# Performance work log

Measured on AMD Instinct MI355X. Metric: run time of the kernel, lower is better.

Reference implementation:

```python
import jax, jax.numpy as jnp
import numpy as np

B, S, C, H = 2, 2048, 2048, 16
Dh = C // H
ROPE_THETA = 10000.0


def _rope(t):
    # t: [B, S, H, Dh]; rotate-half RoPE over head_dim
    half = Dh // 2
    inv_freq = 1.0 / (ROPE_THETA ** (jnp.arange(0, half, dtype=jnp.float32) / half))
    ang = jnp.arange(S, dtype=jnp.float32)[:, None] * inv_freq[None, :]  # [S, half]
    cos = jnp.cos(ang)[None, :, None, :]  # [1,S,1,half]
    sin = jnp.sin(ang)[None, :, None, :]
    t1, t2 = t[..., :half], t[..., half:]
    return jnp.concatenate([t1 * cos - t2 * sin, t2 * cos + t1 * sin], axis=-1)


def setup_inputs() -> dict:
    key = jax.random.key(0)
    k1, k2, k3 = jax.random.split(key, 3)
    x = jax.random.normal(k1, (B, S, C), dtype=jnp.float32)
    Wqkv = jax.random.normal(k2, (C, 3 * C), dtype=jnp.float32) * (C ** -0.5)
    Wproj = jax.random.normal(k3, (C, C), dtype=jnp.float32) * (C ** -0.5)
    return {"x": x, "Wqkv": Wqkv, "Wproj": Wproj}


def reference(x, Wqkv, Wproj):
    batch, seq, hidden = x.shape
    qkv = x @ Wqkv  # [B,S,3C]
    # NOTE: torch code chunks as k, q, v (k first)
    k, q, v = jnp.split(qkv, 3, axis=-1)
    k = k.reshape(batch, seq, H, Dh)
    q = q.reshape(batch, seq, H, Dh)
    v = v.reshape(batch, seq, H, Dh)
    k = _rope(k)
    q = _rope(q)
    scale = Dh ** -0.5
    scores = jnp.einsum('bqhd,bkhd->bhqk', q, k) * scale  # [B,H,S,S]
    causal = jnp.tril(jnp.ones((seq, seq), dtype=bool))
    scores = jnp.where(causal[None, None], scores, jnp.finfo(scores.dtype).min)
    attn = jax.nn.softmax(scores, axis=-1)
    out = jnp.einsum('bhqk,bkhd->bqhd', attn, v).reshape(batch, seq, hidden)
    return out @ Wproj
```

## Files before the change

kernel.cpp:

```cpp
#include <hip/hip_runtime.h>
#include <hip/hip_bf16.h>

#define B_   2
#define S_   2048
#define C_   2048
#define H_   16
#define DH   128
#define C3   (3 * C_)

typedef __attribute__((ext_vector_type(8))) short short8;
typedef __attribute__((ext_vector_type(4))) float floatx4;

__device__ __forceinline__ void gload16(const void* g, void* l) {
  __builtin_amdgcn_global_load_lds(
      (const __attribute__((address_space(1))) unsigned int*)g,
      (__attribute__((address_space(3))) unsigned int*)l, 16, 0, 0);
}

__device__ __forceinline__ unsigned pk_bf16(float a, float b) {
  union { __hip_bfloat16 h; unsigned short u; } ua, ub;
  ua.h = __float2bfloat16(a); ub.h = __float2bfloat16(b);
  return (unsigned)ua.u | ((unsigned)ub.u << 16);
}

__device__ __forceinline__ float bf2f(short u) {
  union { unsigned u; float f; } t;
  t.u = ((unsigned)(unsigned short)u) << 16;
  return t.f;
}
__device__ __forceinline__ short f2bf(float f) {
  union { __hip_bfloat16 h; short s; } t;
  t.h = __float2bfloat16(f);
  return t.s;
}

__device__ __forceinline__ void transpose_cast_dev(
    const float* __restrict__ in, __hip_bfloat16* __restrict__ out,
    int R, int Cc, int c0, int r0, int tid, float (*tile)[33]) {
  int row = tid >> 3, col4 = tid & 7;
  float4 v = *(const float4*)&in[(size_t)(r0 + row) * Cc + c0 + col4 * 4];
  tile[row][col4 * 4 + 0] = v.x;
  tile[row][col4 * 4 + 1] = v.y;
  tile[row][col4 * 4 + 2] = v.z;
  tile[row][col4 * 4 + 3] = v.w;
  __syncthreads();
  int c = tid >> 3, r4 = tid & 7;
  union { __hip_bfloat16 b[4]; uint2 u; } t;
#pragma unroll
  for (int e = 0; e < 4; ++e) t.b[e] = __float2bfloat16(tile[r4 * 4 + e][c]);
  *(uint2*)&out[(size_t)(c0 + c) * R + r0 + r4 * 4] = t.u;
}

__global__ __launch_bounds__(256) void pre_kernel(
    const float* __restrict__ x, __hip_bfloat16* __restrict__ xb,
    const float* __restrict__ Wqkv, __hip_bfloat16* __restrict__ WqkvT) {
  __shared__ float tile[32][33];
  const int bid = blockIdx.x, tid = threadIdx.x;
  if (bid < 8192) {
    int i = bid * 256 + tid;
    float4 v = ((const float4*)x)[i];
    union { __hip_bfloat16 b[4]; uint2 u; } t;
    t.b[0] = __float2bfloat16(v.x);
    t.b[1] = __float2bfloat16(v.y);
    t.b[2] = __float2bfloat16(v.z);
    t.b[3] = __float2bfloat16(v.w);
    ((uint2*)xb)[i] = t.u;
  } else {
    int tb = bid - 8192;
    int bx = tb % 192, by = tb / 192;
    transpose_cast_dev(Wqkv, WqkvT, 2048, 6144, bx * 32, by * 32, tid, tile);
  }
}

#define S_VMCNT2 do { asm volatile("s_waitcnt vmcnt(2)" ::: "memory"); \
                      __builtin_amdgcn_sched_barrier(0); } while (0)
#define S_LGKM0  do { asm volatile("s_waitcnt lgkmcnt(0)" ::: "memory"); \
                      __builtin_amdgcn_sched_barrier(0); } while (0)
#define S_BAR    do { __builtin_amdgcn_s_barrier(); \
                      __builtin_amdgcn_sched_barrier(0); } while (0)


#define RD_A4(dst, buf, mh, sl)                                                          \
  do {                                                                                   \
    const __hip_bfloat16* base_ =                                                        \
        lds + (buf) * 28672 + (wm * 128 + (mh) * 64 + lr) * 64 + ((sl) ? sw1 : sw0);     \
    _Pragma("unroll") for (int i_ = 0; i_ < 4; ++i_)                                     \
        dst[i_] = *(const short8*)(base_ + i_ * 1024);                                   \
  } while (0)

#define RD_B3(dst, buf, sl)                                                              \
  do {                                                                                   \
    const __hip_bfloat16* base_ =                                                        \
        lds + (buf) * 28672 + 16384 + (wn * 48 + lr) * 64 + ((sl) ? sw1 : sw0);          \
    _Pragma("unroll") for (int j_ = 0; j_ < 3; ++j_)                                     \
        dst[j_] = *(const short8*)(base_ + j_ * 1024);                                   \
  } while (0)

#define MFG(afp, bfp, mh)                                                                \
  do {                                                                                   \
    __builtin_amdgcn_s_setprio(1);                                                       \
    _Pragma("unroll") for (int i_ = 0; i_ < 4; ++i_)                                     \
    _Pragma("unroll") for (int j_ = 0; j_ < 3; ++j_)                                     \
        acc[(mh) * 4 + i_][j_] = __builtin_amdgcn_mfma_f32_16x16x32_bf16(                \
            afp[i_], bfp[j_], acc[(mh) * 4 + i_][j_], 0, 0, 0);                          \
    __builtin_amdgcn_s_setprio(0);                                                       \
  } while (0)

__global__ __launch_bounds__(512, 2) void gemm1_kernel(
    const __hip_bfloat16* __restrict__ A, const __hip_bfloat16* __restrict__ Bt,
    __hip_bfloat16* __restrict__ Cp) {
  const int K = 2048;
  __shared__ __hip_bfloat16 lds[2 * 28672];
  const int tid = threadIdx.x;
  const int lane = tid & 63, wv = tid >> 6;
  const int wm = wv >> 2, wn = wv & 3;
  const int lr = lane & 15, lq = lane >> 4;
  const int m0 = blockIdx.y * 256, n0 = blockIdx.x * 192;
  const int sw0 = (lq ^ (lr & 7)) << 3;
  const int sw1 = sw0 ^ 32;

  const __hip_bfloat16* Abase = A + (size_t)m0 * K;
  const __hip_bfloat16* Bbase = Bt + (size_t)n0 * K;

  auto stA = [&](int buf, int half, int kk) {
#pragma unroll
    for (int pp = 0; pp < 2; ++pp) {
      int p = half * 2 + pp;
      int idx = p * 512 + tid;
      int row = idx >> 3;
      int lc = (idx & 7) ^ (row & 7);
      gload16(Abase + (size_t)row * K + kk + lc * 8,
              (char*)lds + buf * 57344 + p * 8192 + wv * 1024);
    }
  };
  auto stB2 = [&](int buf, int kk) {
#pragma unroll
    for (int p = 0; p < 2; ++p) {
      int idx = p * 512 + tid;
      int row = idx >> 3;
      int lc = (idx & 7) ^ (row & 7);
      gload16(Bbase + (size_t)row * K + kk + lc * 8,
              (char*)lds + buf * 57344 + 32768 + p * 8192 + wv * 1024);
    }
  };
  auto stB1 = [&](int buf, int kk) {
    int idx = 2 * 512 + tid;
    int row = idx >> 3;
    int lc = (idx & 7) ^ (row & 7);
    gload16(Bbase + (size_t)row * K + kk + lc * 8,
            (char*)lds + buf * 57344 + 49152 + wv * 1024);
  };

  floatx4 acc[8][3] = {};
  short8 afA[4], afB[4], afC[4], afD[4], bfA[3], bfB[3];

  stA(0, 0, 0); stA(0, 1, 0); stB2(0, 0); stB1(0, 0);
  stA(1, 0, 64);

#pragma unroll 1
  for (int it = 0; it < 16; ++it) {
    const int t = 2 * it;
    const int kk1 = (t + 1) * 64;
    const int kk2 = (t + 2 < 32) ? (t + 2) * 64 : 0;
    const int kk3 = (t + 3 < 32) ? (t + 3) * 64 : 0;

    S_VMCNT2; S_BAR;
    RD_A4(afA, 0, 0, 0); RD_B3(bfA, 0, 0);
    stA(1, 1, kk1);
    S_LGKM0;
    MFG(afA, bfA, 0);
    S_BAR;
    RD_A4(afB, 0, 1, 0); RD_A4(afC, 0, 0, 1);
    stB2(1, kk1);
    S_LGKM0;
    MFG(afB, bfA, 1);
    S_BAR;
    RD_B3(bfB, 0, 1); RD_A4(afD, 0, 1, 1);
    stB1(1, kk1);
    S_LGKM0;
    MFG(afC, bfB, 0);
    S_BAR;
    stA(0, 0, kk2);
    MFG(afD, bfB, 1);
    S_BAR;

    S_VMCNT2; S_BAR;
    RD_A4(afA, 1, 0, 0); RD_B3(bfA, 1, 0);
    stA(0, 1, kk2);
    S_LGKM0;
    MFG(afA, bfA, 0);
    S_BAR;
    RD_A4(afB, 1, 1, 0); RD_A4(afC, 1, 0, 1);
    stB2(0, kk2);
    S_LGKM0;
    MFG(afB, bfA, 1);
    S_BAR;
    RD_B3(bfB, 1, 1); RD_A4(afD, 1, 1, 1);
    stB1(0, kk2);
    S_LGKM0;
    MFG(afC, bfB, 0);
    S_BAR;
    stA(1, 0, kk3);
    MFG(afD, bfB, 1);
    S_BAR;
  }

  asm volatile("s_waitcnt vmcnt(0)" ::: "memory");
  __builtin_amdgcn_sched_barrier(0);

#pragma unroll
  for (int i = 0; i < 8; ++i)
#pragma unroll
    for (int j = 0; j < 3; ++j)
#pragma unroll
      for (int r = 0; r < 4; ++r) {
        int row = m0 + wm * 128 + i * 16 + lq * 4 + r;
        int col = n0 + wn * 48 + j * 16 + lr;
        Cp[(size_t)row * 6144 + col] = __float2bfloat16(acc[i][j][r]);
      }
}

#define S_VMCNT6 do { asm volatile("s_waitcnt vmcnt(6)" ::: "memory"); \
                      __builtin_amdgcn_sched_barrier(0); } while (0)

template <int NCOLS, bool OUT_F32>
__global__ __launch_bounds__(512, 2) void gemm_dp_kernel(
    const __hip_bfloat16* __restrict__ A, const __hip_bfloat16* __restrict__ Bt,
    void* __restrict__ Cp) {
  const int K = 2048, NT = 32;
  __shared__ __hip_bfloat16 lds[3 * 24576];
  const int tid = threadIdx.x;
  const int lane = tid & 63, wv = tid >> 6;
  const int wm = wv >> 1, wn = wv & 1;
  const int lr = lane & 15, lq = lane >> 4;
  const int m0 = blockIdx.y * 256, n0 = blockIdx.x * 128;
  const int sw0 = (lq ^ (lr & 7)) << 3;
  const int sw1 = sw0 ^ 32;

  auto stageA = [&](int bw, int p, int kk) {
    int idx = p * 512 + tid;
    int row = idx >> 3;
    int lc = (idx & 7) ^ (row & 7);
    gload16(A + (size_t)(m0 + row) * K + kk + lc * 8,
            (char*)lds + (size_t)bw * 49152 + (size_t)(p * 512 + wv * 64) * 16);
  };
  auto stageB = [&](int bw, int p, int kk) {
    int idx = p * 512 + tid;
    int row = idx >> 3;
    int lc = (idx & 7) ^ (row & 7);
    gload16(Bt + (size_t)(n0 + row) * K + kk + lc * 8,
            (char*)lds + (size_t)bw * 49152 + 32768 + (size_t)(p * 512 + wv * 64) * 16);
  };

#pragma unroll
  for (int p = 0; p < 4; ++p) stageA(0, p, 0);
#pragma unroll
  for (int p = 0; p < 2; ++p) stageB(0, p, 0);
#pragma unroll
  for (int p = 0; p < 4; ++p) stageA(1, p, 64);
#pragma unroll
  for (int p = 0; p < 2; ++p) stageB(1, p, 64);

  floatx4 acc[4][4] = {};
  int br = 0, bw = 2;

#pragma unroll 1
  for (int t = 0; t < NT; ++t) {
    const int kk2 = (t + 2 < NT) ? (t + 2) * 64 : 0;

    S_VMCNT6;
    S_BAR;

    const __hip_bfloat16* Ab = lds + br * 24576 + (wm * 64 + lr) * 64;
    const __hip_bfloat16* Bb = lds + br * 24576 + 16384 + (wn * 64 + lr) * 64;

    short8 af0[4], bf0[4];
#pragma unroll
    for (int i = 0; i < 4; ++i) af0[i] = *(const short8*)(Ab + i * 1024 + sw0);
#pragma unroll
    for (int j = 0; j < 4; ++j) bf0[j] = *(const short8*)(Bb + j * 1024 + sw0);
    stageA(bw, 0, kk2); stageA(bw, 1, kk2); stageB(bw, 0, kk2);
    S_LGKM0;
    __builtin_amdgcn_s_setprio(1);
#pragma unroll
    for (int i = 0; i < 4; ++i)
#pragma unroll
      for (int j = 0; j < 4; ++j)
        acc[i][j] = __builtin_amdgcn_mfma_f32_16x16x32_bf16(af0[i], bf0[j], acc[i][j], 0, 0, 0);
    __builtin_amdgcn_s_setprio(0);

    short8 af1[4], bf1[4];
#pragma unroll
    for (int i = 0; i < 4; ++i) af1[i] = *(const short8*)(Ab + i * 1024 + sw1);
#pragma unroll
    for (int j = 0; j < 4; ++j) bf1[j] = *(const short8*)(Bb + j * 1024 + sw1);
    stageA(bw, 2, kk2); stageA(bw, 3, kk2); stageB(bw, 1, kk2);
    S_LGKM0;
    __builtin_amdgcn_s_setprio(1);
#pragma unroll
    for (int i = 0; i < 4; ++i)
#pragma unroll
      for (int j = 0; j < 4; ++j)
        acc[i][j] = __builtin_amdgcn_mfma_f32_16x16x32_bf16(af1[i], bf1[j], acc[i][j], 0, 0, 0);
    __builtin_amdgcn_s_setprio(0);

    br = (br == 2) ? 0 : br + 1;
    bw = (bw == 2) ? 0 : bw + 1;
  }

  asm volatile("s_waitcnt vmcnt(0)" ::: "memory");
  __builtin_amdgcn_sched_barrier(0);

#pragma unroll
  for (int i = 0; i < 4; ++i)
#pragma unroll
    for (int j = 0; j < 4; ++j)
#pragma unroll
      for (int r = 0; r < 4; ++r) {
        int row = m0 + wm * 64 + i * 16 + lq * 4 + r;
        int col = n0 + wn * 64 + j * 16 + lr;
        if (OUT_F32)
          ((float*)Cp)[(size_t)row * NCOLS + col] = acc[i][j][r];
        else
          ((__hip_bfloat16*)Cp)[(size_t)row * NCOLS + col] = __float2bfloat16(acc[i][j][r]);
      }
}

__global__ __launch_bounds__(256) void mid_kernel(
    __hip_bfloat16* __restrict__ qkv, __hip_bfloat16* __restrict__ vt,
    const float* __restrict__ Wproj, __hip_bfloat16* __restrict__ WprojT) {
  __shared__ char smem[18432];
  const int bid = blockIdx.x, tid = threadIdx.x;

  if (bid < 2048) {
    int i = bid * 256 + tid;
    int d8 = (i & 7) << 3;
    int h = (i >> 3) & 15;
    int row = i >> 7;
    int s = row & (S_ - 1);
    size_t base = (size_t)row * C3 + h * DH + d8;
    short8 k1 = *(const short8*)(qkv + base);
    short8 k2 = *(const short8*)(qkv + base + 64);
    short8 q1 = *(const short8*)(qkv + base + C_);
    short8 q2 = *(const short8*)(qkv + base + C_ + 64);
    short8 ko1, ko2, qo1, qo2;
    const float scale = 0.08838834764831845f * 1.4426950408889634f;
#pragma unroll
    for (int j = 0; j < 8; ++j) {
      float invf = exp2f((float)(d8 + j) * (-13.287712379549449f / 64.0f));
      float ang = (float)s * invf;
      float sn, c;
      __sincosf(ang, &sn, &c);
      float a = bf2f(k1[j]), b = bf2f(k2[j]);
      ko1[j] = f2bf(a * c - b * sn);
      ko2[j] = f2bf(b * c + a * sn);
      a = bf2f(q1[j]); b = bf2f(q2[j]);
      qo1[j] = f2bf((a * c - b * sn) * scale);
      qo2[j] = f2bf((b * c + a * sn) * scale);
    }
    *(short8*)(qkv + base) = ko1;
    *(short8*)(qkv + base + 64) = ko2;
    *(short8*)(qkv + base + C_) = qo1;
    *(short8*)(qkv + base + C_ + 64) = qo2;
  } else if (bid < 3072) {
    short* T = (short*)smem;
    const int t = (bid - 2048) & 31, bh = (bid - 2048) >> 5;
    const int b = bh >> 4, h = bh & 15;
    const size_t brow = (size_t)b * S_;
#pragma unroll
    for (int p = 0; p < 4; ++p) {
      int idx = p * 256 + tid;
      int row = idx >> 4, c8 = idx & 15;
      *(short8*)(T + row * 144 + c8 * 8) =
          *(const short8*)(qkv + (brow + t * 64 + row) * C3 + 2 * C_ + h * DH + c8 * 8);
    }
    __syncthreads();
#pragma unroll
    for (int p = 0; p < 4; ++p) {
      int L = p * 256 + tid;
      int d = L & 127, cs = L >> 7;
      short8 v;
#pragma unroll
      for (int j = 0; j < 8; ++j) v[j] = T[(cs * 8 + j) * 144 + d];
      *(short8*)(vt + ((size_t)bh * 32 + t) * 8192 + (size_t)L * 8) = v;
    }
  } else {
    int tb = bid - 3072;
    int bx = tb & 63, by = tb >> 6;
    transpose_cast_dev(Wproj, WprojT, 2048, 2048, bx * 32, by * 32, tid,
                       (float(*)[33])smem);
  }
}

__global__ __launch_bounds__(256, 2) void attn_kernel(
    const __hip_bfloat16* __restrict__ qkv,
    const __hip_bfloat16* __restrict__ vt_tiles,
    __hip_bfloat16* __restrict__ outp) {
  __shared__ __hip_bfloat16 Ks[2][8192];
  __shared__ __hip_bfloat16 Vt[2][8192];

  const int tid = threadIdx.x, lane = tid & 63, wv = tid >> 6;
  const int lr = lane & 15, lq = lane >> 4;
  const int n = blockIdx.y * 16 + blockIdx.x;
  const int half = n >> 8, rr = n & 255;
  const int bh = rr >> 3, p = rr & 7;
  const int qt = half ? p : 15 - p;
  const int b = bh >> 4, h = bh & 15;
  const int q0w = qt * 128 + wv * 32;
  const size_t brow = (size_t)b * S_;
  const int nkt = 2 * qt + 2;
  const int wrow_last = q0w + 31;

  short8 qf[2][4];
#pragma unroll
  for (int rt = 0; rt < 2; ++rt)
#pragma unroll
    for (int ks = 0; ks < 4; ++ks)
      qf[rt][ks] = *(const short8*)(qkv + (brow + q0w + rt * 16 + lr) * C3 + C_ + h * DH + ks * 32 + lq * 8);

  short8 kreg[4], vreg[4];
  auto issue = [&](int kti) {
    if (kti >= nkt) kti = nkt - 1;
    const int kb = kti * 64;
#pragma unroll
    for (int pp = 0; pp < 4; ++pp) {
      int L = pp * 256 + tid;
      int srow = L >> 4;
      int ck = (L & 15) ^ (srow & 15);
      kreg[pp] = *(const short8*)(qkv + (brow + kb + srow) * C3 + h * DH + ck * 8);
      vreg[pp] = *(const short8*)(vt_tiles + ((size_t)bh * 32 + kti) * 8192 + (size_t)L * 8);
    }
  };
  auto commit = [&](int buf) {
#pragma unroll
    for (int pp = 0; pp < 4; ++pp) {
      *(short8*)(Ks[buf] + (size_t)(pp * 256 + tid) * 8) = kreg[pp];
      *(short8*)(Vt[buf] + (size_t)(pp * 256 + tid) * 8) = vreg[pp];
    }
  };

  floatx4 of[2][8] = {};
  float l_run[2] = {0.0f, 0.0f};

  issue(0);
  commit(0);
  __syncthreads();

  for (int kt = 0; kt < nkt; ++kt) {
    const int kb = kt * 64;
    const int buf = kt & 1;
    issue(kt + 1);

    if (kb <= wrow_last) {
      floatx4 st[2][4] = {};
#pragma unroll
      for (int ks = 0; ks < 4; ++ks) {
        short8 kfr[4];
#pragma unroll
        for (int t4 = 0; t4 < 4; ++t4)
          kfr[t4] = *(const short8*)(Ks[buf] + ((t4 * 16 + lr) * 16 + ((ks * 4 + lq) ^ lr)) * 8);
#pragma unroll
        for (int rt = 0; rt < 2; ++rt)
#pragma unroll
          for (int t4 = 0; t4 < 4; ++t4)
            st[rt][t4] = __builtin_amdgcn_mfma_f32_16x16x32_bf16(kfr[t4], qf[rt][ks], st[rt][t4], 0, 0, 0);
      }

      if (kb + 63 > q0w) {
#pragma unroll
        for (int rt = 0; rt < 2; ++rt)
#pragma unroll
          for (int t4 = 0; t4 < 4; ++t4)
#pragma unroll
            for (int r = 0; r < 4; ++r) {
              int s = kb + t4 * 16 + lq * 4 + r;
              if (s > q0w + rt * 16 + lr) st[rt][t4][r] = -1e30f;
            }
      }

#pragma unroll
      for (int rt = 0; rt < 2; ++rt) {
        float rs = 0.0f;
#pragma unroll
        for (int t4 = 0; t4 < 4; ++t4)
#pragma unroll
          for (int r = 0; r < 4; ++r) {
            float pv = exp2f(st[rt][t4][r]);
            st[rt][t4][r] = pv;
            rs += pv;
          }
        rs += __shfl_xor(rs, 16);
        rs += __shfl_xor(rs, 32);
        l_run[rt] += rs;
      }

      unsigned pkL[2][4], pkH[2][4];
#pragma unroll
      for (int rt = 0; rt < 2; ++rt)
#pragma unroll
        for (int t4 = 0; t4 < 4; ++t4) {
          pkL[rt][t4] = pk_bf16(st[rt][t4][0], st[rt][t4][1]);
          pkH[rt][t4] = pk_bf16(st[rt][t4][2], st[rt][t4][3]);
        }
      const int s0 = (lq & 1) * 32 + lr;
      const int s1 = s0 + 16;
      const bool hi = (lq >> 1) != 0;

#pragma unroll
      for (int ks = 0; ks < 2; ++ks) {
        short8 pa[2];
#pragma unroll
        for (int rt = 0; rt < 2; ++rt) {
          unsigned aL0 = __shfl(pkL[rt][2 * ks], s0), aL1 = __shfl(pkL[rt][2 * ks + 1], s0);
          unsigned aH0 = __shfl(pkH[rt][2 * ks], s0), aH1 = __shfl(pkH[rt][2 * ks + 1], s0);
          unsigned bL0 = __shfl(pkL[rt][2 * ks], s1), bL1 = __shfl(pkL[rt][2 * ks + 1], s1);
          unsigned bH0 = __shfl(pkH[rt][2 * ks], s1), bH1 = __shfl(pkH[rt][2 * ks + 1], s1);
          union { unsigned u[4]; short8 v; } pu;
          pu.u[0] = hi ? aL1 : aL0;
          pu.u[1] = hi ? aH1 : aH0;
          pu.u[2] = hi ? bL1 : bL0;
          pu.u[3] = hi ? bH1 : bH0;
          pa[rt] = pu.v;
        }
#pragma unroll
        for (int dt = 0; dt < 8; ++dt) {
          short8 vb = *(const short8*)(Vt[buf] + ((ks * 4 + lq) * 128 + dt * 16 + lr) * 8);
#pragma unroll
          for (int rt = 0; rt < 2; ++rt)
            of[rt][dt] = __builtin_amdgcn_mfma_f32_16x16x32_bf16(pa[rt], vb, of[rt][dt], 0, 0, 0);
        }
      }
    }

    commit(buf ^ 1);
    __syncthreads();
  }

#pragma unroll
  for (int rt = 0; rt < 2; ++rt) {
    float linv = 1.0f / l_run[rt];
    floatx4 lv;
#pragma unroll
    for (int r = 0; r < 4; ++r) lv[r] = __shfl(linv, lq * 4 + r);
#pragma unroll
    for (int dt = 0; dt < 8; ++dt)
#pragma unroll
      for (int r = 0; r < 4; ++r)
        outp[(brow + q0w + rt * 16 + lq * 4 + r) * C_ + h * DH + dt * 16 + lr] =
            __float2bfloat16(of[rt][dt][r] * lv[r]);
  }
}

extern "C" void kernel_launch(void* const* d_in, const int* in_sizes, int n_in,
                              void* d_out, int out_size, void* d_ws, size_t ws_size,
                              hipStream_t stream) {
  const float* x = (const float*)d_in[0];
  const float* Wqkv = (const float*)d_in[1];
  const float* Wproj = (const float*)d_in[2];

  __hip_bfloat16* xb = (__hip_bfloat16*)d_ws;
  __hip_bfloat16* WqkvT = xb + (size_t)4096 * 2048;
  __hip_bfloat16* qkvb = WqkvT + (size_t)6144 * 2048;
  __hip_bfloat16* WprojT = WqkvT;
  __hip_bfloat16* vt_tiles = WqkvT + (size_t)2048 * 2048;
  __hip_bfloat16* attnb = xb;

  pre_kernel<<<8192 + 12288, 256, 0, stream>>>(x, xb, Wqkv, WqkvT);

  gemm1_kernel<<<dim3(6144 / 192, 4096 / 256), 512, 0, stream>>>(xb, WqkvT, qkvb);

  mid_kernel<<<2048 + 1024 + 4096, 256, 0, stream>>>(qkvb, vt_tiles, Wproj, WprojT);

  attn_kernel<<<dim3(16, 32), 256, 0, stream>>>(qkvb, vt_tiles, attnb);

  gemm_dp_kernel<2048, true><<<dim3(2048 / 128, 4096 / 256), 512, 0, stream>>>(
      attnb, WprojT, (float*)d_out);
}
```

Before: 345.4 us.

## Move Wproj transpose into pre kernel, enlarge transpose tiles, swizzle Vt LDS

```diff
diff --git a/kernel.cpp b/kernel.cpp
--- a/kernel.cpp
+++ b/kernel.cpp
@@ -34,27 +34,34 @@
   return t.s;
 }
 
-__device__ __forceinline__ void transpose_cast_dev(
+__device__ __forceinline__ void transpose_cast_dev64(
     const float* __restrict__ in, __hip_bfloat16* __restrict__ out,
-    int R, int Cc, int c0, int r0, int tid, float (*tile)[33]) {
-  int row = tid >> 3, col4 = tid & 7;
-  float4 v = *(const float4*)&in[(size_t)(r0 + row) * Cc + c0 + col4 * 4];
-  tile[row][col4 * 4 + 0] = v.x;
-  tile[row][col4 * 4 + 1] = v.y;
-  tile[row][col4 * 4 + 2] = v.z;
-  tile[row][col4 * 4 + 3] = v.w;
+    int R, int Cc, int c0, int r0, int tid, float (*T)[33]) {
+#pragma unroll
+  for (int pass = 0; pass < 2; ++pass) {
+    int row = pass * 32 + (tid >> 3), c4 = tid & 7;
+    float4 v = *(const float4*)&in[(size_t)(r0 + row) * Cc + c0 + c4 * 4];
+    T[row][c4 * 4 + 0] = v.x;
+    T[row][c4 * 4 + 1] = v.y;
+    T[row][c4 * 4 + 2] = v.z;
+    T[row][c4 * 4 + 3] = v.w;
+  }
   __syncthreads();
-  int c = tid >> 3, r4 = tid & 7;
-  union { __hip_bfloat16 b[4]; uint2 u; } t;
-#pragma unroll
-  for (int e = 0; e < 4; ++e) t.b[e] = __float2bfloat16(tile[r4 * 4 + e][c]);
-  *(uint2*)&out[(size_t)(c0 + c) * R + r0 + r4 * 4] = t.u;
+#pragma unroll
+  for (int pass = 0; pass < 2; ++pass) {
+    int oc = pass * 16 + (tid >> 4), rq = tid & 15;
+    union { __hip_bfloat16 b[4]; uint2 u; } t;
+#pragma unroll
+    for (int e = 0; e < 4; ++e) t.b[e] = __float2bfloat16(T[rq * 4 + e][oc]);
+    *(uint2*)&out[(size_t)(c0 + oc) * R + r0 + rq * 4] = t.u;
+  }
 }
 
 __global__ __launch_bounds__(256) void pre_kernel(
     const float* __restrict__ x, __hip_bfloat16* __restrict__ xb,
-    const float* __restrict__ Wqkv, __hip_bfloat16* __restrict__ WqkvT) {
-  __shared__ float tile[32][33];
+    const float* __restrict__ Wqkv, __hip_bfloat16* __restrict__ WqkvT,
+    const float* __restrict__ Wproj, __hip_bfloat16* __restrict__ WprojT) {
+  __shared__ float tile[64][33];
   const int bid = blockIdx.x, tid = threadIdx.x;
   if (bid < 8192) {
     int i = bid * 256 + tid;
@@ -65,10 +72,14 @@
     t.b[2] = __float2bfloat16(v.z);
     t.b[3] = __float2bfloat16(v.w);
     ((uint2*)xb)[i] = t.u;
-  } else {
+  } else if (bid < 14336) {
     int tb = bid - 8192;
     int bx = tb % 192, by = tb / 192;
-    transpose_cast_dev(Wqkv, WqkvT, 2048, 6144, bx * 32, by * 32, tid, tile);
+    transpose_cast_dev64(Wqkv, WqkvT, 2048, 6144, bx * 32, by * 64, tid, tile);
+  } else {
+    int tb = bid - 14336;
+    int bx = tb & 63, by = tb >> 6;
+    transpose_cast_dev64(Wproj, WprojT, 2048, 2048, bx * 32, by * 64, tid, tile);
   }
 }
 
@@ -327,9 +338,8 @@
 }
 
 __global__ __launch_bounds__(256) void mid_kernel(
-    __hip_bfloat16* __restrict__ qkv, __hip_bfloat16* __restrict__ vt,
-    const float* __restrict__ Wproj, __hip_bfloat16* __restrict__ WprojT) {
-  __shared__ char smem[18432];
+    __hip_bfloat16* __restrict__ qkv, __hip_bfloat16* __restrict__ vt) {
+  __shared__ short T[64 * 144];
   const int bid = blockIdx.x, tid = threadIdx.x;
 
   if (bid < 2048) {
@@ -362,8 +372,7 @@
     *(short8*)(qkv + base + 64) = ko2;
     *(short8*)(qkv + base + C_) = qo1;
     *(short8*)(qkv + base + C_ + 64) = qo2;
-  } else if (bid < 3072) {
-    short* T = (short*)smem;
+  } else {
     const int t = (bid - 2048) & 31, bh = (bid - 2048) >> 5;
     const int b = bh >> 4, h = bh & 15;
     const size_t brow = (size_t)b * S_;
@@ -384,11 +393,6 @@
       for (int j = 0; j < 8; ++j) v[j] = T[(cs * 8 + j) * 144 + d];
       *(short8*)(vt + ((size_t)bh * 32 + t) * 8192 + (size_t)L * 8) = v;
     }
-  } else {
-    int tb = bid - 3072;
-    int bx = tb & 63, by = tb >> 6;
-    transpose_cast_dev(Wproj, WprojT, 2048, 2048, bx * 32, by * 32, tid,
-                       (float(*)[33])smem);
   }
 }
 
@@ -434,8 +438,10 @@
   auto commit = [&](int buf) {
 #pragma unroll
     for (int pp = 0; pp < 4; ++pp) {
-      *(short8*)(Ks[buf] + (size_t)(pp * 256 + tid) * 8) = kreg[pp];
-      *(short8*)(Vt[buf] + (size_t)(pp * 256 + tid) * 8) = vreg[pp];
+      int Lw = pp * 256 + tid;
+      int pw = Lw ^ ((Lw >> 7) & 7);
+      *(short8*)(Ks[buf] + (size_t)Lw * 8) = kreg[pp];
+      *(short8*)(Vt[buf] + (size_t)pw * 8) = vreg[pp];
     }
   };
 
@@ -522,9 +528,11 @@
           pu.u[3] = hi ? bH1 : bH0;
           pa[rt] = pu.v;
         }
+        const int cs = ks * 4 + lq;
+        const int vx = lr ^ (cs & 7);
 #pragma unroll
         for (int dt = 0; dt < 8; ++dt) {
-          short8 vb = *(const short8*)(Vt[buf] + ((ks * 4 + lq) * 128 + dt * 16 + lr) * 8);
+          short8 vb = *(const short8*)(Vt[buf] + (cs * 128 + dt * 16 + vx) * 8);
 #pragma unroll
           for (int rt = 0; rt < 2; ++rt)
             of[rt][dt] = __builtin_amdgcn_mfma_f32_16x16x32_bf16(pa[rt], vb, of[rt][dt], 0, 0, 0);
@@ -561,15 +569,15 @@
   __hip_bfloat16* xb = (__hip_bfloat16*)d_ws;
   __hip_bfloat16* WqkvT = xb + (size_t)4096 * 2048;
   __hip_bfloat16* qkvb = WqkvT + (size_t)6144 * 2048;
-  __hip_bfloat16* WprojT = WqkvT;
-  __hip_bfloat16* vt_tiles = WqkvT + (size_t)2048 * 2048;
+  __hip_bfloat16* WprojT = qkvb + (size_t)4096 * 6144;
+  __hip_bfloat16* vt_tiles = WqkvT;
   __hip_bfloat16* attnb = xb;
 
-  pre_kernel<<<8192 + 12288, 256, 0, stream>>>(x, xb, Wqkv, WqkvT);
+  pre_kernel<<<16384, 256, 0, stream>>>(x, xb, Wqkv, WqkvT, Wproj, WprojT);
 
   gemm1_kernel<<<dim3(6144 / 192, 4096 / 256), 512, 0, stream>>>(xb, WqkvT, qkvb);
 
-  mid_kernel<<<2048 + 1024 + 4096, 256, 0, stream>>>(qkvb, vt_tiles, Wproj, WprojT);
+  mid_kernel<<<2048 + 1024, 256, 0, stream>>>(qkvb, vt_tiles);
 
   attn_kernel<<<dim3(16, 32), 256, 0, stream>>>(qkvb, vt_tiles, attnb);
 
```

Result: faster. 336.0 us (-2.7%).
